# Optimization experiments

Hardware: AMD Instinct MI355X
Metric: run time of the kernel (lower is better)

## Reference

```python
import jax, jax.numpy as jnp
import numpy as np

B, S, P, D, L = 8, 224, 14, 512, 6
NPS = S // P            # 16 patches per side
N = NPS * NPS           # 256 tokens
G = L - 1               # 5 feedforward groups
H = D * 4
TOKEN_ATTEND_SELF_VALUE = -0.0005


def setup_inputs() -> dict:
    key = jax.random.key(0)
    k = jax.random.split(key, 8)
    s = 0.02
    f = jnp.float32
    return {
        "img": jax.random.normal(k[0], (B, 3, S, S), f),
        "W_patch": jax.random.normal(k[1], (P * P * 3, D), f) * s,
        "b_patch": jnp.zeros((D,), f),
        "pos_emb": jax.random.normal(k[2], (N, D), f) * s,
        "init_levels": jax.random.normal(k[3], (L, D), f),
        "bu_W1": jax.random.normal(k[4], (G, D, H), f) * s,
        "bu_b1": jnp.zeros((G, H), f),
        "bu_W2": jax.random.normal(k[5], (G, H, D), f) * s,
        "bu_b2": jnp.zeros((G, D), f),
        "td_W1": jax.random.normal(k[6], (G, D, H), f) * s,
        "td_b1": jnp.zeros((G, H), f),
        "td_W2": jax.random.normal(k[7], (G, H, D), f) * s,
        "td_b2": jnp.zeros((G, D), f),
        "iters": 12,
    }


def _grouped_ff(x, W1, b1, W2, b2):
    # x: [b, n, G, d]; grouped 1x1 conv == independent per-level MLP
    h = jax.nn.gelu(jnp.einsum('bnld,ldh->bnlh', x, W1) + b1, approximate=False)
    return jnp.einsum('bnlh,lhd->bnld', h, W2) + b2


def _consensus(levels):
    # levels: [b, n, L, d]; q = levels, k = l2-normalized levels, v = levels
    d = levels.shape[-1]
    norm = jnp.maximum(jnp.linalg.norm(levels, axis=-1, keepdims=True), 1e-12)
    k = levels / norm
    sim = jnp.einsum('bild,bjld->blij', levels, k) * (d ** -0.5)
    n = levels.shape[1]
    eye = jnp.eye(n, dtype=bool)[None, None]
    sim = jnp.where(eye, TOKEN_ATTEND_SELF_VALUE, sim)  # attend_self=False
    attn = jax.nn.softmax(sim, axis=-1)
    return jnp.einsum('blij,bjld->bild', attn, levels)


def _forward(img, W_patch, b_patch, pos_emb, init_levels,
             bu_W1, bu_b1, bu_W2, bu_b2, td_W1, td_b1, td_W2, td_b2, iters):
    b = img.shape[0]
    # 'b c (h p1) (w p2) -> b (h w) (p1 p2 c)'
    x = img.reshape(b, 3, NPS, P, NPS, P).transpose(0, 2, 4, 3, 5, 1).reshape(b, N, P * P * 3)
    tokens = x @ W_patch + b_patch                  # [b, n, d]
    bottom = tokens[:, :, None, :]                  # [b, n, 1, d]
    levels = jnp.broadcast_to(init_levels, (b, N, L, D)).astype(img.dtype)
    pos = pos_emb[None, :, None, :]
    contrib = jnp.array([4.0] * (L - 1) + [3.0], jnp.float32).reshape(1, 1, L, 1)

    def step(lv, _):
        lw = jnp.concatenate([bottom, lv], axis=-2)                 # [b, n, L+1, d]
        bu = _grouped_ff(lw[..., 1:-1, :], bu_W1, bu_b1, bu_W2, bu_b2)
        td = _grouped_ff(lw[..., 2:, :] + pos, td_W1, td_b1, td_W2, td_b2)
        bu = jnp.concatenate([bottom, bu], axis=-2)                 # [b, n, L, d]
        td = jnp.pad(td, ((0, 0), (0, 0), (0, 1), (0, 0)))          # [b, n, L, d]
        cons = _consensus(lv)
        new = (lv + bu + td + cons) / contrib
        return new, None

    levels, _ = jax.lax.scan(step, levels, None, length=iters)
    return levels


def reference(img, W_patch, b_patch, pos_emb, init_levels,
              bu_W1, bu_b1, bu_W2, bu_b2, td_W1, td_b1, td_W2, td_b2, iters):
    return _forward(img, W_patch, b_patch, pos_emb, init_levels,
                    bu_W1, bu_b1, bu_W2, bu_b2, td_W1, td_b1, td_W2, td_b2, iters)
```

## Files before the change

kernel.cpp:

```cpp
#include <hip/hip_runtime.h>
#include <math.h>

#define L6 6

typedef __attribute__((ext_vector_type(8))) short bf16x8;
typedef __attribute__((ext_vector_type(4))) float f32x4;

#define SH_W_GRP   2097152ull
#define SH_A_TDOFF 10485760ull

__device__ __forceinline__ float gelu_exact(float x) {
  return 0.5f * x * (1.0f + erff(x * 0.70710678118654752f));
}

__device__ __forceinline__ unsigned short bf16_rn(float x) {
  unsigned u = __float_as_uint(x);
  unsigned r = u + 0x7FFFu + ((u >> 16) & 1u);
  return (unsigned short)(r >> 16);
}
__device__ __forceinline__ float bf16_f(unsigned short h) {
  return __uint_as_float(((unsigned)h) << 16);
}
__device__ __forceinline__ void split2(float x, unsigned short* h, unsigned short* l) {
  unsigned short hh = bf16_rn(x);
  *h = hh;
  *l = bf16_rn(x - bf16_f(hh));
}
__device__ __forceinline__ int4 pack8(const unsigned short* v) {
  return make_int4((int)((unsigned)v[0] | ((unsigned)v[1] << 16)),
                   (int)((unsigned)v[2] | ((unsigned)v[3] << 16)),
                   (int)((unsigned)v[4] | ((unsigned)v[5] << 16)),
                   (int)((unsigned)v[6] | ((unsigned)v[7] << 16)));
}

__device__ __forceinline__ void gload16(const void* g, void* l) {
  __builtin_amdgcn_global_load_lds(
      (const __attribute__((address_space(1))) void*)g,
      (__attribute__((address_space(3))) void*)l, 16, 0, 0);
}

__device__ __forceinline__ void patch_embed_body(
    char* smem, const float* __restrict__ img, const float* __restrict__ Wp,
    const float* __restrict__ bp, float* __restrict__ tokens, int bn8)
{
  float (*xs)[588] = (float(*)[588])smem;
  float (*part)[8][4] = (float(*)[8][4])(smem + 18816);
  const int tid = threadIdx.x;
  for (int e = tid; e < 4704; e += 256) {
    int p = e / 588, k = e - p * 588;
    int m = bn8 * 8 + p;
    int b = m >> 8, n = m & 255;
    int i = n >> 4, j = n & 15;
    int c = k % 3;
    int t = k / 3;
    int pc = t % 14;
    int pr = t / 14;
    xs[p][k] = img[(((size_t)(b * 3 + c) * 224) + (i * 14 + pr)) * 224 + (j * 14 + pc)];
  }
  __syncthreads();
  const int kh = tid >> 7, dq = tid & 127, d0 = dq * 4;
  float acc[8][4];
#pragma unroll
  for (int p = 0; p < 8; ++p)
#pragma unroll
    for (int i = 0; i < 4; ++i) acc[p][i] = 0.f;
  const int kbeg = kh * 294;
  for (int k = kbeg; k < kbeg + 294; ++k) {
    float4 wv = *(const float4*)(Wp + (size_t)k * 512 + d0);
#pragma unroll
    for (int p = 0; p < 8; ++p) {
      float x = xs[p][k];
      acc[p][0] = fmaf(x, wv.x, acc[p][0]);
      acc[p][1] = fmaf(x, wv.y, acc[p][1]);
      acc[p][2] = fmaf(x, wv.z, acc[p][2]);
      acc[p][3] = fmaf(x, wv.w, acc[p][3]);
    }
  }
  if (kh == 0) {
#pragma unroll
    for (int p = 0; p < 8; ++p)
      *(float4*)&part[dq][p][0] =
          make_float4(acc[p][0], acc[p][1], acc[p][2], acc[p][3]);
  }
  __syncthreads();
  if (kh == 1) {
    float4 bv = *(const float4*)(bp + d0);
#pragma unroll
    for (int p = 0; p < 8; ++p) {
      int m = bn8 * 8 + p;
      float4 o = make_float4(part[dq][p][0] + acc[p][0] + bv.x,
                             part[dq][p][1] + acc[p][1] + bv.y,
                             part[dq][p][2] + acc[p][2] + bv.z,
                             part[dq][p][3] + acc[p][3] + bv.w);
      *(float4*)(tokens + (size_t)m * 512 + d0) = o;
    }
  }
}

__device__ __forceinline__ void init_lv_body(
    const float* __restrict__ initl, float* __restrict__ lv, int bidx)
{
  int f = bidx * 256 + threadIdx.x;
  int d4 = f & 127;
  int l = (f >> 15) % 6;
  float4 v = *(const float4*)(initl + (size_t)l * 512 + d4 * 4);
  *(float4*)(lv + (size_t)f * 4) = v;
}

__device__ __forceinline__ void pack_w_body(
    const float* __restrict__ src, short* __restrict__ dst, int KT, int NT,
    int inner)
{
  int sidx = inner * 256 + threadIdx.x;
  int slot = sidx & 511;
  int blk = sidx >> 9;
  int kt = blk % KT;
  int rest = blk / KT;
  int nt = rest % NT;
  int g = rest / NT;
  int f = slot >> 6, lane = slot & 63;
  int N = NT * 128, K = KT * 32;
  int n = nt * 128 + f * 16 + (lane & 15);
  int k0 = kt * 32 + (lane >> 4) * 8;
  const float* s = src + ((size_t)g * K + k0) * N + n;
  unsigned short hi[8], lo[8];
#pragma unroll
  for (int j = 0; j < 8; ++j) split2(s[(size_t)j * N], &hi[j], &lo[j]);
  short* d = dst + (size_t)blk * 8192 + slot * 8;
  *(int4*)d = pack8(hi);
  *(int4*)(d + 4096) = pack8(lo);
}

__global__ __launch_bounds__(256) void startup1(
    const float* __restrict__ buW1, const float* __restrict__ tdW1,
    const float* __restrict__ buW2, const float* __restrict__ tdW2,
    short* __restrict__ W1all, short* __restrict__ W2all,
    const float* __restrict__ img, const float* __restrict__ Wp,
    const float* __restrict__ bp, float* __restrict__ tokens,
    const float* __restrict__ initl, float* __restrict__ lv)
{
  __shared__ __align__(16) char smem[35200];
  const int bx = blockIdx.x;
  if (bx < 10240) {
    int q = bx / 2560;
    int inner = bx - q * 2560;
    const float* src = (q == 0) ? buW1 : (q == 1) ? tdW1 : (q == 2) ? buW2 : tdW2;
    short* dst = (q == 0) ? W1all
               : (q == 1) ? W1all + 5 * SH_W_GRP
               : (q == 2) ? W2all
                          : W2all + 5 * SH_W_GRP;
    int KT = (q < 2) ? 16 : 64;
    int NT = (q < 2) ? 16 : 4;
    pack_w_body(src, dst, KT, NT, inner);
  } else if (bx < 10496) {
    patch_embed_body(smem, img, Wp, bp, tokens, bx - 10240);
  } else {
    init_lv_body(initl, lv, bx - 10496);
  }
}

__global__ __launch_bounds__(256) void startup2(
    const float* __restrict__ lv, float* __restrict__ invn,
    const float* __restrict__ pos, short* __restrict__ Abu,
    short* __restrict__ Atd)
{
  if (blockIdx.x < 48) {
    int bl = blockIdx.x;
    int n = threadIdx.x;
    const float* row = lv + ((size_t)bl * 256 + n) * 512;
    float ss = 0.f;
    for (int k = 0; k < 512; k += 4) {
      float4 v = *(const float4*)(row + k);
      ss = fmaf(v.x, v.x, ss);
      ss = fmaf(v.y, v.y, ss);
      ss = fmaf(v.z, v.z, ss);
      ss = fmaf(v.w, v.w, ss);
    }
    invn[(size_t)bl * 256 + n] = 1.0f / fmaxf(sqrtf(ss), 1e-12f);
    return;
  }
  const int bx = blockIdx.x - 48;
  const int lg = bx >> 8, mt = (bx >> 4) & 15, kt = bx & 15;
  const size_t blk = (size_t)bx * 8192;
#pragma unroll
  for (int ss = 0; ss < 2; ++ss) {
    int s = threadIdx.x + ss * 256;
    int f = s >> 6, l = s & 63;
    int m = mt * 128 + (f << 4) + (l & 15);
    int b = m >> 8, n = m & 255;
    int d = kt * 32 + ((l >> 4) << 3);
    const float* pbu = lv + ((size_t)(b * L6 + lg) * 256 + n) * 512 + d;
    const float* ptd = lv + ((size_t)(b * L6 + lg + 1) * 256 + n) * 512 + d;
    const float* pp = pos + (size_t)n * 512 + d;
    float4 u0 = *(const float4*)pbu;
    float4 u1 = *(const float4*)(pbu + 4);
    float xv[8] = {u0.x, u0.y, u0.z, u0.w, u1.x, u1.y, u1.z, u1.w};
    unsigned short hi[8], lo[8];
#pragma unroll
    for (int j = 0; j < 8; ++j) split2(xv[j], &hi[j], &lo[j]);
    *(int4*)(Abu + blk + s * 8) = pack8(hi);
    *(int4*)(Abu + blk + 4096 + s * 8) = pack8(lo);
    float4 v0 = *(const float4*)ptd;
    float4 v1 = *(const float4*)(ptd + 4);
    float4 p0 = *(const float4*)pp;
    float4 p1 = *(const float4*)(pp + 4);
    float yv[8] = {v0.x + p0.x, v0.y + p0.y, v0.z + p0.z, v0.w + p0.w,
                   v1.x + p1.x, v1.y + p1.y, v1.z + p1.z, v1.w + p1.w};
#pragma unroll
    for (int j = 0; j < 8; ++j) split2(yv[j], &hi[j], &lo[j]);
    *(int4*)(Atd + blk + s * 8) = pack8(hi);
    *(int4*)(Atd + blk + 4096 + s * 8) = pack8(lo);
  }
}

__device__ __forceinline__ void ff1_body(
    const short* __restrict__ Wa, const short* __restrict__ Ap,
    const float* __restrict__ b1, short* __restrict__ hpk, int gid)
{
  const int tt = gid & 15;
  const int tile = gid >> 4;
  const int ht = tile & 15;
  const int z = tile >> 4;
  const int tid = threadIdx.x, lane = tid & 63, w = tid >> 6;
  const int wm = (w >> 1) * 64, wn = (w & 1) * 64;
  const short* ga = Wa + (size_t)(z * 16 + ht) * 16 * 8192 + (wm << 5) + lane * 8;
  const short* gb = Ap + (size_t)(z * 16 + tt) * 16 * 8192 + (wn << 5) + lane * 8;

  f32x4 acc[4][4];
#pragma unroll
  for (int i = 0; i < 4; ++i)
#pragma unroll
    for (int j = 0; j < 4; ++j) acc[i][j] = (f32x4)(0.0f);

  for (int kt = 0; kt < 16; ++kt) {
    const short* pa = ga + (size_t)kt * 8192;
    const short* pb = gb + (size_t)kt * 8192;
    bf16x8 ah[4], al[4], bh[4], bl[4];
#pragma unroll
    for (int i = 0; i < 4; ++i) {
      ah[i] = *(const bf16x8*)(pa + i * 512);
      al[i] = *(const bf16x8*)(pa + 4096 + i * 512);
    }
#pragma unroll
    for (int j = 0; j < 4; ++j) {
      bh[j] = *(const bf16x8*)(pb + j * 512);
      bl[j] = *(const bf16x8*)(pb + 4096 + j * 512);
    }
#pragma unroll
    for (int j = 0; j < 4; ++j)
#pragma unroll
      for (int i = 0; i < 4; ++i)
        acc[i][j] = __builtin_amdgcn_mfma_f32_16x16x32_bf16(
            ah[i], bh[j], acc[i][j], 0, 0, 0);
#pragma unroll
    for (int j = 0; j < 4; ++j)
#pragma unroll
      for (int i = 0; i < 4; ++i)
        acc[i][j] = __builtin_amdgcn_mfma_f32_16x16x32_bf16(
            al[i], bh[j], acc[i][j], 0, 0, 0);
#pragma unroll
    for (int j = 0; j < 4; ++j)
#pragma unroll
      for (int i = 0; i < 4; ++i)
        acc[i][j] = __builtin_amdgcn_mfma_f32_16x16x32_bf16(
            ah[i], bl[j], acc[i][j], 0, 0, 0);
  }

  const int q = lane >> 4, t = lane & 15;
  const float* b1g = b1 + (size_t)z * 2048;
#pragma unroll
  for (int i = 0; i < 4; ++i) {
    int Hb = ht * 128 + wm + i * 16 + q * 4;
    float4 bv = *(const float4*)(b1g + Hb);
    float bb[4] = {bv.x, bv.y, bv.z, bv.w};
    int kt2 = Hb >> 5;
    int g2 = (Hb >> 3) & 3;
    int jb = Hb & 7;
    size_t blkbase = ((size_t)(z * 16 + tt) * 64 + kt2) * 4096;
#pragma unroll
    for (int j = 0; j < 4; ++j) {
      int f2 = (wn >> 4) + j;
      size_t off = blkbase + (size_t)(f2 * 64 + g2 * 16 + t) * 8 + jb;
      unsigned short hi[4];
#pragma unroll
      for (int r = 0; r < 4; ++r)
        hi[r] = bf16_rn(gelu_exact(acc[i][j][r] + bb[r]));
      *(uint2*)(hpk + off) =
          make_uint2((unsigned)hi[0] | ((unsigned)hi[1] << 16),
                     (unsigned)hi[2] | ((unsigned)hi[3] << 16));
    }
  }
}

__device__ __forceinline__ void ff2_body(
    char* smem, const short* __restrict__ hpk, const short* __restrict__ Wb,
    const float* __restrict__ b2, const float* __restrict__ lv,
    const float* __restrict__ tokens, float* __restrict__ accum,
    int olvbase, int emode, int gid)
{
  short* SA = (short*)smem;
  short* SB = (short*)(smem + 4096);
  const int nt2 = gid & 3;
  const int tile = gid >> 2;
  const int mt2 = tile & 31;
  const int z = tile >> 5;

  const int tid = threadIdx.x, lane = tid & 63, w = tid >> 6;
  const int wm = (w >> 1) * 32, wn = (w & 1) * 64;
  const short* gaBase = hpk + (size_t)(z * 16 + (mt2 >> 1)) * 64 * 4096
                        + (size_t)(mt2 & 1) * 2048;
  const short* gb = Wb + (size_t)(z * 4 + nt2) * 64 * 8192;

  f32x4 acc[2][4];
#pragma unroll
  for (int i = 0; i < 2; ++i)
#pragma unroll
    for (int j = 0; j < 4; ++j) acc[i][j] = (f32x4)(0.0f);

  for (int kt = 0; kt < 64; ++kt) {
    __syncthreads();
    const char* pa = (const char*)(gaBase + (size_t)kt * 4096);
    const char* pb = (const char*)(gb + (size_t)kt * 8192);
    gload16(pa + w * 1024 + lane * 16, (char*)SA + w * 1024);
#pragma unroll
    for (int c = 0; c < 4; ++c)
      gload16(pb + w * 4096 + c * 1024 + lane * 16,
              (char*)SB + w * 4096 + c * 1024);
    __syncthreads();
    bf16x8 ah[2];
#pragma unroll
    for (int i = 0; i < 2; ++i) {
      int f = (wm >> 4) + i;
      ah[i] = *(const bf16x8*)&SA[f * 512 + lane * 8];
    }
#pragma unroll
    for (int jp = 0; jp < 2; ++jp) {
      bf16x8 bh[2], bl[2];
#pragma unroll
      for (int j2 = 0; j2 < 2; ++j2) {
        int f = (wn >> 4) + jp * 2 + j2;
        bh[j2] = *(const bf16x8*)&SB[f * 512 + lane * 8];
        bl[j2] = *(const bf16x8*)&SB[4096 + f * 512 + lane * 8];
      }
#pragma unroll
      for (int j2 = 0; j2 < 2; ++j2)
#pragma unroll
        for (int i = 0; i < 2; ++i)
          acc[i][jp * 2 + j2] = __builtin_amdgcn_mfma_f32_16x16x32_bf16(
              ah[i], bh[j2], acc[i][jp * 2 + j2], 0, 0, 0);
#pragma unroll
      for (int j2 = 0; j2 < 2; ++j2)
#pragma unroll
        for (int i = 0; i < 2; ++i)
          acc[i][jp * 2 + j2] = __builtin_amdgcn_mfma_f32_16x16x32_bf16(
              ah[i], bl[j2], acc[i][jp * 2 + j2], 0, 0, 0);
    }
  }

  const int q = lane >> 4, t = lane & 15;
  const float* b2g = b2 + (size_t)z * 512;
  const int level = olvbase + z;
#pragma unroll
  for (int i = 0; i < 2; ++i) {
#pragma unroll
    for (int r = 0; r < 4; ++r) {
      int m = mt2 * 64 + wm + i * 16 + q * 4 + r;
      int b = m >> 8, n = m & 255;
      size_t rowoff = ((size_t)(b * L6 + level) * 256 + n) * 512;
      float* arow = accum + rowoff;
      const float* lrow = lv + rowoff;
      const float* trow = tokens + (size_t)m * 512;
#pragma unroll
      for (int j = 0; j < 4; ++j) {
        int col = nt2 * 128 + wn + j * 16 + t;
        float v = acc[i][j][r] + b2g[col];
        if (emode == 0)                       arow[col] = lrow[col] + v;
        else if (level == 0)                  arow[col] = lrow[col] + trow[col] + v;
        else                                  arow[col] += v;
      }
    }
  }
}

__device__ __forceinline__ void attn_body(
    char* smem, const float* __restrict__ lv, const short* __restrict__ Apk,
    const float* __restrict__ invn, float* __restrict__ attnb, int a)
{
  short* Bhi = (short*)smem;
  short* Blo = (short*)(smem + 16384);
  float* scL = (float*)(smem + 32768);
  float (*red)[4] = (float(*)[4])(smem + 33792);
  const int s = a >> 3;
  const int b = a & 7;
  const int l = s >> 3;
  const int bl = b * 6 + l;
  const int i0 = (s & 7) * 32;
  const float* base = lv + (size_t)bl * 131072;
  const int tid = threadIdx.x, lane = tid & 63, w = tid >> 6;
  const int q = lane >> 4, c = lane & 15;

  scL[tid] = invn[(size_t)bl * 256 + tid];

  f32x4 acc[2][4];
#pragma unroll
  for (int i = 0; i < 2; ++i)
#pragma unroll
    for (int j = 0; j < 4; ++j) acc[i][j] = (f32x4)(0.0f);

  const short* src0 = Apk + ((size_t)(l * 16 + 2 * b) * 16) * 8192;
  const short* src1 = Apk + ((size_t)(l * 16 + 2 * b + 1) * 16) * 8192;

  for (int kt = 0; kt < 16; ++kt) {
    __syncthreads();
    if (l < 5) {
      const char* p0 = (const char*)(src0 + (size_t)kt * 8192);
      const char* p1 = (const char*)(src1 + (size_t)kt * 8192);
      gload16(p0 + tid * 16,         (char*)Bhi + tid * 16);
      gload16(p0 + 4096 + tid * 16,  (char*)Bhi + 4096 + tid * 16);
      gload16(p0 + 8192 + tid * 16,  (char*)Blo + tid * 16);
      gload16(p0 + 12288 + tid * 16, (char*)Blo + 4096 + tid * 16);
      gload16(p1 + tid * 16,         (char*)Bhi + 8192 + tid * 16);
      gload16(p1 + 4096 + tid * 16,  (char*)Bhi + 12288 + tid * 16);
      gload16(p1 + 8192 + tid * 16,  (char*)Blo + 8192 + tid * 16);
      gload16(p1 + 12288 + tid * 16, (char*)Blo + 12288 + tid * 16);
    } else {
      const int k0 = kt * 32;
#pragma unroll
      for (int it = 0; it < 8; ++it) {
        int f = it * 256 + tid;
        int j = f >> 3, c4 = f & 7;
        float4 v = *(const float4*)(base + (size_t)j * 512 + k0 + c4 * 4);
        unsigned short hi[4], lo[4];
        split2(v.x, &hi[0], &lo[0]);
        split2(v.y, &hi[1], &lo[1]);
        split2(v.z, &hi[2], &lo[2]);
        split2(v.w, &hi[3], &lo[3]);
        int fg = j >> 4;
        int la = (c4 >> 1) * 16 + (j & 15);
        int half = (c4 & 1) * 4;
        *(uint2*)&Bhi[fg * 512 + la * 8 + half] =
            make_uint2((unsigned)hi[0] | ((unsigned)hi[1] << 16),
                       (unsigned)hi[2] | ((unsigned)hi[3] << 16));
        *(uint2*)&Blo[fg * 512 + la * 8 + half] =
            make_uint2((unsigned)lo[0] | ((unsigned)lo[1] << 16),
                       (unsigned)lo[2] | ((unsigned)lo[3] << 16));
      }
    }
    __syncthreads();
    bf16x8 ah[2], al[2], bh[4], blv[4];
#pragma unroll
    for (int i = 0; i < 2; ++i) {
      int fg = (i0 >> 4) + i;
      ah[i] = *(const bf16x8*)&Bhi[fg * 512 + lane * 8];
      al[i] = *(const bf16x8*)&Blo[fg * 512 + lane * 8];
    }
#pragma unroll
    for (int j = 0; j < 4; ++j) {
      int fg = w * 4 + j;
      bh[j] = *(const bf16x8*)&Bhi[fg * 512 + lane * 8];
      blv[j] = *(const bf16x8*)&Blo[fg * 512 + lane * 8];
    }
#pragma unroll
    for (int j = 0; j < 4; ++j)
#pragma unroll
      for (int i = 0; i < 2; ++i)
        acc[i][j] = __builtin_amdgcn_mfma_f32_16x16x32_bf16(
            ah[i], bh[j], acc[i][j], 0, 0, 0);
#pragma unroll
    for (int j = 0; j < 4; ++j)
#pragma unroll
      for (int i = 0; i < 2; ++i)
        acc[i][j] = __builtin_amdgcn_mfma_f32_16x16x32_bf16(
            al[i], bh[j], acc[i][j], 0, 0, 0);
#pragma unroll
    for (int j = 0; j < 4; ++j)
#pragma unroll
      for (int i = 0; i < 2; ++i)
        acc[i][j] = __builtin_amdgcn_mfma_f32_16x16x32_bf16(
            ah[i], blv[j], acc[i][j], 0, 0, 0);
  }
  __syncthreads();

  const float rs = 0.04419417382415922f;
#pragma unroll
  for (int ai = 0; ai < 2; ++ai)
#pragma unroll
    for (int bj = 0; bj < 4; ++bj)
#pragma unroll
      for (int r = 0; r < 4; ++r) {
        int i = i0 + ai * 16 + q * 4 + r;
        int j = w * 64 + bj * 16 + c;
        float sv = acc[ai][bj][r] * scL[j] * rs;
        if (j == i) sv = -0.0005f;
        acc[ai][bj][r] = sv;
      }
  float mx[2][4];
#pragma unroll
  for (int ai = 0; ai < 2; ++ai)
#pragma unroll
    for (int r = 0; r < 4; ++r) {
      float m = fmaxf(fmaxf(acc[ai][0][r], acc[ai][1][r]),
                      fmaxf(acc[ai][2][r], acc[ai][3][r]));
      m = fmaxf(m, __shfl_xor(m, 1));
      m = fmaxf(m, __shfl_xor(m, 2));
      m = fmaxf(m, __shfl_xor(m, 4));
      m = fmaxf(m, __shfl_xor(m, 8));
      mx[ai][r] = m;
    }
  if (c == 0) {
#pragma unroll
    for (int ai = 0; ai < 2; ++ai)
#pragma unroll
      for (int r = 0; r < 4; ++r) red[ai * 16 + q * 4 + r][w] = mx[ai][r];
  }
  __syncthreads();
#pragma unroll
  for (int ai = 0; ai < 2; ++ai)
#pragma unroll
    for (int r = 0; r < 4; ++r) {
      int row = ai * 16 + q * 4 + r;
      mx[ai][r] = fmaxf(fmaxf(red[row][0], red[row][1]),
                        fmaxf(red[row][2], red[row][3]));
    }
  __syncthreads();
  float sm[2][4];
#pragma unroll
  for (int ai = 0; ai < 2; ++ai)
#pragma unroll
    for (int r = 0; r < 4; ++r) {
      float t = 0.f;
#pragma unroll
      for (int bj = 0; bj < 4; ++bj) {
        float e = expf(acc[ai][bj][r] - mx[ai][r]);
        acc[ai][bj][r] = e;
        t += e;
      }
      t += __shfl_xor(t, 1);
      t += __shfl_xor(t, 2);
      t += __shfl_xor(t, 4);
      t += __shfl_xor(t, 8);
      sm[ai][r] = t;
    }
  if (c == 0) {
#pragma unroll
    for (int ai = 0; ai < 2; ++ai)
#pragma unroll
      for (int r = 0; r < 4; ++r) red[ai * 16 + q * 4 + r][w] = sm[ai][r];
  }
  __syncthreads();
  float* ob = attnb + (size_t)bl * 65536;
#pragma unroll
  for (int ai = 0; ai < 2; ++ai)
#pragma unroll
    for (int r = 0; r < 4; ++r) {
      int row = ai * 16 + q * 4 + r;
      float S = red[row][0] + red[row][1] + red[row][2] + red[row][3];
      float inv = 1.0f / S;
      int i = i0 + row;
#pragma unroll
      for (int bj = 0; bj < 4; ++bj) {
        int j = w * 64 + bj * 16 + c;
        ob[(size_t)i * 256 + j] = acc[ai][bj][r] * inv;
      }
    }
}

__global__ __launch_bounds__(256, 3) void ff1_k(
    const short* __restrict__ Wa, const short* __restrict__ Ap,
    const float* __restrict__ b1, short* __restrict__ hpk)
{
  const int per_x = gridDim.x >> 3;
  const int gid = (blockIdx.x & 7) * per_x + (blockIdx.x >> 3);
  ff1_body(Wa, Ap, b1, hpk, gid);
}

__global__ __launch_bounds__(256, 3) void k_ff2bu_ff1td(
    const short* __restrict__ hallbu, const short* __restrict__ W2,
    const float* __restrict__ bub2, const float* __restrict__ lv,
    const float* __restrict__ tokens, float* __restrict__ accum,
    const short* __restrict__ W1td, const short* __restrict__ Atd,
    const float* __restrict__ tdb1, short* __restrict__ halltd)
{
  __shared__ __align__(16) char smem[20480];
  if (blockIdx.x < 640) {
    int bid = blockIdx.x;
    int gid = (bid & 7) * 80 + (bid >> 3);
    ff2_body(smem, hallbu, W2, bub2, lv, tokens, accum, 1, 0, gid);
  } else {
    int bid = blockIdx.x - 640;
    int gid = (bid & 7) * 160 + (bid >> 3);
    ff1_body(W1td, Atd, tdb1, halltd, gid);
  }
}

__global__ __launch_bounds__(256, 3) void k_ff2td_attn(
    const short* __restrict__ halltd, const short* __restrict__ W2td,
    const float* __restrict__ tdb2, const float* __restrict__ lv,
    const float* __restrict__ tokens, float* __restrict__ accum,
    const short* __restrict__ Apk, const float* __restrict__ invn,
    float* __restrict__ attnb)
{
  __shared__ __align__(16) char smem[34304];
  if (blockIdx.x < 640) {
    int bid = blockIdx.x;
    int gid = (bid & 7) * 80 + (bid >> 3);
    ff2_body(smem, halltd, W2td, tdb2, lv, tokens, accum, 0, 1, gid);
  } else {
    attn_body(smem, lv, Apk, invn, attnb, blockIdx.x - 640);
  }
}

__global__ __launch_bounds__(256) void cons_k(
    const float* __restrict__ attnb, const float* __restrict__ lv,
    float* __restrict__ accum)
{
  __shared__ __align__(16) char smemraw[25088];
  const int a = blockIdx.x;
  const int s = a >> 3;
  const int bl = (a & 7) * 6 + (s >> 4);
  const int tile = s & 15;
  int it0 = (tile >> 2) * 64;
  int dt0 = (tile & 3) * 128;
  const float* A = attnb + (size_t)bl * 65536;
  const float* Bm = lv + (size_t)bl * 131072;
  float (*Ast)[68] = (float(*)[68])smemraw;
  float (*Bs)[128] = (float(*)[128])(smemraw + 8704);
  const int tid = threadIdx.x;
  const int ty = tid >> 4, tx = tid & 15;
  float acc[4][8];
#pragma unroll
  for (int i = 0; i < 4; ++i)
#pragma unroll
    for (int j = 0; j < 8; ++j) acc[i][j] = 0.f;

  for (int k0 = 0; k0 < 256; k0 += 32) {
#pragma unroll
    for (int it = 0; it < 2; ++it) {
      int f = it * 256 + tid;
      int r = f >> 3, c4 = f & 7;
      float4 v = *(const float4*)(A + (size_t)(it0 + r) * 256 + k0 + c4 * 4);
      Ast[c4 * 4 + 0][r] = v.x;
      Ast[c4 * 4 + 1][r] = v.y;
      Ast[c4 * 4 + 2][r] = v.z;
      Ast[c4 * 4 + 3][r] = v.w;
    }
#pragma unroll
    for (int it = 0; it < 4; ++it) {
      int kr = (tid >> 5) + it * 8;
      int c4 = tid & 31;
      *(float4*)&Bs[kr][c4 * 4] =
          *(const float4*)(Bm + (size_t)(k0 + kr) * 512 + dt0 + c4 * 4);
    }
    __syncthreads();
#pragma unroll 8
    for (int k = 0; k < 32; ++k) {
      float4 av = *(const float4*)&Ast[k][ty * 4];
      float4 b0 = *(const float4*)&Bs[k][tx * 4];
      float4 b1 = *(const float4*)&Bs[k][64 + tx * 4];
      float avv[4] = {av.x, av.y, av.z, av.w};
      float bv[8] = {b0.x, b0.y, b0.z, b0.w, b1.x, b1.y, b1.z, b1.w};
#pragma unroll
      for (int i = 0; i < 4; ++i)
#pragma unroll
        for (int j = 0; j < 8; ++j)
          acc[i][j] = fmaf(avv[i], bv[j], acc[i][j]);
    }
    __syncthreads();
  }
#pragma unroll
  for (int ii = 0; ii < 4; ++ii) {
    int i = it0 + ty * 4 + ii;
    float* arow = accum + (size_t)bl * 131072 + (size_t)i * 512 + dt0;
#pragma unroll
    for (int j = 0; j < 4; ++j) arow[tx * 4 + j] += acc[ii][j];
#pragma unroll
    for (int j = 0; j < 4; ++j) arow[64 + tx * 4 + j] += acc[ii][4 + j];
  }
}

__global__ __launch_bounds__(256) void combine3(
    const float* __restrict__ accum, const float* __restrict__ pos,
    float* __restrict__ lv_out, short* __restrict__ Abu,
    short* __restrict__ Atd, float* __restrict__ invn,
    float* __restrict__ dout, int last)
{
  int t = blockIdx.x * 256 + threadIdx.x;
  int d8 = t & 63;
  int n = (t >> 6) & 255;
  int v = t >> 14;
  int l = v % 6, b = v / 6;
  int bn = (b << 8) | n;
  size_t idx = ((size_t)v * 256 + n) * 512 + d8 * 8;
  float4 a0 = *(const float4*)(accum + idx);
  float4 a1 = *(const float4*)(accum + idx + 4);
  float sc = (l == 5) ? (1.0f / 3.0f) : 0.25f;
  float r[8];
  r[0] = a0.x * sc; r[1] = a0.y * sc; r[2] = a0.z * sc; r[3] = a0.w * sc;
  r[4] = a1.x * sc; r[5] = a1.y * sc; r[6] = a1.z * sc; r[7] = a1.w * sc;
  *(float4*)(lv_out + idx) = make_float4(r[0], r[1], r[2], r[3]);
  *(float4*)(lv_out + idx + 4) = make_float4(r[4], r[5], r[6], r[7]);
  if (last) {
    float* dp = dout + ((size_t)bn * 6 + l) * 512 + d8 * 8;
    *(float4*)dp = make_float4(r[0], r[1], r[2], r[3]);
    *(float4*)(dp + 4) = make_float4(r[4], r[5], r[6], r[7]);
  }
  {
    float s8 = 0.f;
#pragma unroll
    for (int j = 0; j < 8; ++j) s8 = fmaf(r[j], r[j], s8);
#pragma unroll
    for (int o = 1; o < 64; o <<= 1) s8 += __shfl_xor(s8, o);
    if (d8 == 0) invn[(size_t)v * 256 + n] = 1.0f / fmaxf(sqrtf(s8), 1e-12f);
  }
  int m = bn;
  int mt = m >> 7;
  int kt = d8 >> 2;
  int s = (((m & 127) >> 4) << 6) | (((d8 & 3) << 4) | (m & 15));
  unsigned short hi[8], lo[8];
  if (l < 5) {
    size_t blk = ((size_t)(l * 16 + mt) * 16 + kt) * 8192;
#pragma unroll
    for (int j = 0; j < 8; ++j) split2(r[j], &hi[j], &lo[j]);
    *(int4*)(Abu + blk + s * 8) = pack8(hi);
    *(int4*)(Abu + blk + 4096 + s * 8) = pack8(lo);
  }
  if (l >= 1) {
    const float* pp = pos + (size_t)n * 512 + d8 * 8;
    float4 p0 = *(const float4*)pp;
    float4 p1 = *(const float4*)(pp + 4);
    float y[8] = {r[0] + p0.x, r[1] + p0.y, r[2] + p0.z, r[3] + p0.w,
                  r[4] + p1.x, r[5] + p1.y, r[6] + p1.z, r[7] + p1.w};
    size_t blk = ((size_t)((l - 1) * 16 + mt) * 16 + kt) * 8192;
#pragma unroll
    for (int j = 0; j < 8; ++j) split2(y[j], &hi[j], &lo[j]);
    *(int4*)(Atd + blk + s * 8) = pack8(hi);
    *(int4*)(Atd + blk + 4096 + s * 8) = pack8(lo);
  }
}

extern "C" void kernel_launch(void* const* d_in, const int* in_sizes, int n_in,
                              void* d_out, int out_size, void* d_ws, size_t ws_size,
                              hipStream_t stream)
{
  const float* img   = (const float*)d_in[0];
  const float* Wp    = (const float*)d_in[1];
  const float* bp    = (const float*)d_in[2];
  const float* pos   = (const float*)d_in[3];
  const float* initl = (const float*)d_in[4];
  const float* buW1  = (const float*)d_in[5];
  const float* bub1  = (const float*)d_in[6];
  const float* buW2  = (const float*)d_in[7];
  const float* bub2  = (const float*)d_in[8];
  const float* tdW1  = (const float*)d_in[9];
  const float* tdb1  = (const float*)d_in[10];
  const float* tdW2  = (const float*)d_in[11];
  const float* tdb2  = (const float*)d_in[12];

  float* ws = (float*)d_ws;
  const size_t LV = (size_t)8 * 6 * 256 * 512;
  float* lv     = ws;
  float* tokens = lv + LV;
  float* accum  = tokens + 1048576ull;
  short* W1all  = (short*)(accum + LV);
  short* W2all  = W1all + 20971520ull;
  short* Apk    = W2all + 20971520ull;
  short* hallbu = Apk + 20971520ull;
  short* halltd = hallbu + 20971520ull;
  float* invn   = (float*)(halltd + 20971520ull);

  float* attnb = (float*)hallbu;
  float* dout  = (float*)d_out;

  startup1<<<16640, 256, 0, stream>>>(buW1, tdW1, buW2, tdW2, W1all, W2all,
                                      img, Wp, bp, tokens, initl, lv);
  startup2<<<1328, 256, 0, stream>>>(lv, invn, pos, Apk, Apk + SH_A_TDOFF);

  for (int it = 0; it < 12; ++it) {
    ff1_k<<<1280, 256, 0, stream>>>(W1all, Apk, bub1, hallbu);
    k_ff2bu_ff1td<<<1920, 256, 0, stream>>>(
        hallbu, W2all, bub2, lv, tokens, accum,
        W1all + 5 * SH_W_GRP, Apk + SH_A_TDOFF, tdb1, halltd);
    k_ff2td_attn<<<1024, 256, 0, stream>>>(
        halltd, W2all + 5 * SH_W_GRP, tdb2, lv, tokens, accum,
        Apk, invn, attnb);
    cons_k<<<768, 256, 0, stream>>>(attnb, lv, accum);
    combine3<<<3072, 256, 0, stream>>>(accum, pos, lv, Apk, Apk + SH_A_TDOFF,
                                       invn, dout, it == 11 ? 1 : 0);
  }
}
```

Baseline: 3.915 ms.

## Re-slice per-iteration kernels into six diagonal stages mixing levels across phases

Splits each iteration's work into six launches where different level groups run at different phases: bu FF1 for levels 0-2, then FF1 for levels 3-4 together with FF2 for levels 0-1 and td FF1, and so on through consensus and combine. The goal is to balance block counts per launch and overlap compute-heavy GEMMs with memory-bound consensus and combine work, shrinking idle tails. The cost is one more launch per iteration, plus correctness that depends on a subtle cross-level dependency ordering. For example, combine for some levels runs while consensus for others is still pending, and it overwrites lv and Abu/Atd that later stages read.

```diff
diff --git a/kernel.cpp b/kernel.cpp
--- a/kernel.cpp
+++ b/kernel.cpp
@@ -215,12 +215,12 @@
 
 __device__ __forceinline__ void ff1_body(
     const short* __restrict__ Wa, const short* __restrict__ Ap,
-    const float* __restrict__ b1, short* __restrict__ hpk, int gid)
+    const float* __restrict__ b1, short* __restrict__ hpk, int gid, int zoff)
 {
   const int tt = gid & 15;
   const int tile = gid >> 4;
   const int ht = tile & 15;
-  const int z = tile >> 4;
+  const int z = zoff + (tile >> 4);
   const int tid = threadIdx.x, lane = tid & 63, w = tid >> 6;
   const int wm = (w >> 1) * 64, wn = (w & 1) * 64;
   const short* ga = Wa + (size_t)(z * 16 + ht) * 16 * 8192 + (wm << 5) + lane * 8;
@@ -296,14 +296,14 @@
     char* smem, const short* __restrict__ hpk, const short* __restrict__ Wb,
     const float* __restrict__ b2, const float* __restrict__ lv,
     const float* __restrict__ tokens, float* __restrict__ accum,
-    int olvbase, int emode, int gid)
+    int olvbase, int emode, int gid, int zoff)
 {
   short* SA = (short*)smem;
   short* SB = (short*)(smem + 4096);
   const int nt2 = gid & 3;
   const int tile = gid >> 2;
   const int mt2 = tile & 31;
-  const int z = tile >> 5;
+  const int z = zoff + (tile >> 5);
 
   const int tid = threadIdx.x, lane = tid & 63, w = tid >> 6;
   const int wm = (w >> 1) * 32, wn = (w & 1) * 64;
@@ -565,66 +565,16 @@
     }
 }
 
-__global__ __launch_bounds__(256, 3) void ff1_k(
-    const short* __restrict__ Wa, const short* __restrict__ Ap,
-    const float* __restrict__ b1, short* __restrict__ hpk)
-{
-  const int per_x = gridDim.x >> 3;
-  const int gid = (blockIdx.x & 7) * per_x + (blockIdx.x >> 3);
-  ff1_body(Wa, Ap, b1, hpk, gid);
-}
-
-__global__ __launch_bounds__(256, 3) void k_ff2bu_ff1td(
-    const short* __restrict__ hallbu, const short* __restrict__ W2,
-    const float* __restrict__ bub2, const float* __restrict__ lv,
-    const float* __restrict__ tokens, float* __restrict__ accum,
-    const short* __restrict__ W1td, const short* __restrict__ Atd,
-    const float* __restrict__ tdb1, short* __restrict__ halltd)
-{
-  __shared__ __align__(16) char smem[20480];
-  if (blockIdx.x < 640) {
-    int bid = blockIdx.x;
-    int gid = (bid & 7) * 80 + (bid >> 3);
-    ff2_body(smem, hallbu, W2, bub2, lv, tokens, accum, 1, 0, gid);
-  } else {
-    int bid = blockIdx.x - 640;
-    int gid = (bid & 7) * 160 + (bid >> 3);
-    ff1_body(W1td, Atd, tdb1, halltd, gid);
-  }
-}
-
-__global__ __launch_bounds__(256, 3) void k_ff2td_attn(
-    const short* __restrict__ halltd, const short* __restrict__ W2td,
-    const float* __restrict__ tdb2, const float* __restrict__ lv,
-    const float* __restrict__ tokens, float* __restrict__ accum,
-    const short* __restrict__ Apk, const float* __restrict__ invn,
-    float* __restrict__ attnb)
-{
-  __shared__ __align__(16) char smem[34304];
-  if (blockIdx.x < 640) {
-    int bid = blockIdx.x;
-    int gid = (bid & 7) * 80 + (bid >> 3);
-    ff2_body(smem, halltd, W2td, tdb2, lv, tokens, accum, 0, 1, gid);
-  } else {
-    attn_body(smem, lv, Apk, invn, attnb, blockIdx.x - 640);
-  }
-}
-
-__global__ __launch_bounds__(256) void cons_k(
-    const float* __restrict__ attnb, const float* __restrict__ lv,
-    float* __restrict__ accum)
-{
-  __shared__ __align__(16) char smemraw[25088];
-  const int a = blockIdx.x;
-  const int s = a >> 3;
-  const int bl = (a & 7) * 6 + (s >> 4);
-  const int tile = s & 15;
+__device__ __forceinline__ void cons_body(
+    char* smem, const float* __restrict__ attnb, const float* __restrict__ lv,
+    float* __restrict__ accum, int bl, int tile)
+{
   int it0 = (tile >> 2) * 64;
   int dt0 = (tile & 3) * 128;
   const float* A = attnb + (size_t)bl * 65536;
   const float* Bm = lv + (size_t)bl * 131072;
-  float (*Ast)[68] = (float(*)[68])smemraw;
-  float (*Bs)[128] = (float(*)[128])(smemraw + 8704);
+  float (*Ast)[68] = (float(*)[68])smem;
+  float (*Bs)[128] = (float(*)[128])(smem + 8704);
   const int tid = threadIdx.x;
   const int ty = tid >> 4, tx = tid & 15;
   float acc[4][8];
@@ -678,17 +628,16 @@
   }
 }
 
-__global__ __launch_bounds__(256) void combine3(
+__device__ __forceinline__ void combine_body(
     const float* __restrict__ accum, const float* __restrict__ pos,
     float* __restrict__ lv_out, short* __restrict__ Abu,
     short* __restrict__ Atd, float* __restrict__ invn,
-    float* __restrict__ dout, int last)
-{
-  int t = blockIdx.x * 256 + threadIdx.x;
-  int d8 = t & 63;
-  int n = (t >> 6) & 255;
-  int v = t >> 14;
-  int l = v % 6, b = v / 6;
+    float* __restrict__ dout, int last, int b, int l, int inner)
+{
+  int f = inner * 256 + threadIdx.x;
+  int d8 = f & 63;
+  int n = f >> 6;
+  int v = b * 6 + l;
   int bn = (b << 8) | n;
   size_t idx = ((size_t)v * 256 + n) * 512 + d8 * 8;
   float4 a0 = *(const float4*)(accum + idx);
@@ -738,6 +687,124 @@
   }
 }
 
+__global__ __launch_bounds__(256, 3) void k_d1(
+    const short* __restrict__ W1bu, const short* __restrict__ Abu,
+    const float* __restrict__ bub1, short* __restrict__ hallbu)
+{
+  const int gid = (blockIdx.x & 7) * 96 + (blockIdx.x >> 3);
+  ff1_body(W1bu, Abu, bub1, hallbu, gid, 0);
+}
+
+__global__ __launch_bounds__(256, 3) void k_d2(
+    const short* __restrict__ W1bu, const short* __restrict__ Abu,
+    const float* __restrict__ bub1, short* __restrict__ hallbu,
+    const short* __restrict__ W2bu, const float* __restrict__ bub2,
+    const float* __restrict__ lv, const float* __restrict__ tokens,
+    float* __restrict__ accum,
+    const short* __restrict__ W1td, const short* __restrict__ Atd,
+    const float* __restrict__ tdb1, short* __restrict__ halltd)
+{
+  __shared__ __align__(16) char smem[20480];
+  const int bx = blockIdx.x;
+  if (bx < 512) {
+    int gid = (bx & 7) * 64 + (bx >> 3);
+    ff1_body(W1bu, Abu, bub1, hallbu, gid, 3);
+  } else if (bx < 768) {
+    int a = bx - 512;
+    int gid = (a & 7) * 32 + (a >> 3);
+    ff2_body(smem, hallbu, W2bu, bub2, lv, tokens, accum, 1, 0, gid, 0);
+  } else {
+    int a = bx - 768;
+    int gid = (a & 7) * 160 + (a >> 3);
+    ff1_body(W1td, Atd, tdb1, halltd, gid, 0);
+  }
+}
+
+__global__ __launch_bounds__(256, 3) void k_d3(
+    const short* __restrict__ hallbu, const short* __restrict__ W2bu,
+    const float* __restrict__ bub2,
+    const short* __restrict__ halltd, const short* __restrict__ W2td,
+    const float* __restrict__ tdb2,
+    const float* __restrict__ lv, const float* __restrict__ tokens,
+    float* __restrict__ accum,
+    const short* __restrict__ Apk, const float* __restrict__ invn,
+    float* __restrict__ attnb)
+{
+  __shared__ __align__(16) char smem[34304];
+  const int bx = blockIdx.x;
+  if (bx < 384) {
+    int gid = (bx & 7) * 48 + (bx >> 3);
+    ff2_body(smem, hallbu, W2bu, bub2, lv, tokens, accum, 1, 0, gid, 2);
+  } else if (bx < 768) {
+    int a = bx - 384;
+    int gid = (a & 7) * 48 + (a >> 3);
+    ff2_body(smem, halltd, W2td, tdb2, lv, tokens, accum, 0, 1, gid, 0);
+  } else {
+    attn_body(smem, lv, Apk, invn, attnb, bx - 768);
+  }
+}
+
+__global__ __launch_bounds__(256, 3) void k_d4(
+    const short* __restrict__ halltd, const short* __restrict__ W2td,
+    const float* __restrict__ tdb2, const float* __restrict__ lv,
+    const float* __restrict__ tokens, float* __restrict__ accum,
+    const float* __restrict__ attnb)
+{
+  __shared__ __align__(16) char smem[25088];
+  const int bx = blockIdx.x;
+  if (bx < 256) {
+    int gid = (bx & 7) * 32 + (bx >> 3);
+    ff2_body(smem, halltd, W2td, tdb2, lv, tokens, accum, 0, 1, gid, 3);
+  } else {
+    int a = bx - 256;
+    int s = a >> 3;
+    int li = s >> 4;
+    int l = (li == 3) ? 5 : li;
+    int bl = (a & 7) * 6 + l;
+    cons_body(smem, attnb, lv, accum, bl, s & 15);
+  }
+}
+
+__global__ __launch_bounds__(256, 3) void k_d5(
+    const float* __restrict__ attnb, const float* __restrict__ lv,
+    float* __restrict__ accum,
+    const float* __restrict__ pos, float* __restrict__ lv_out,
+    short* __restrict__ Abu, short* __restrict__ Atd,
+    float* __restrict__ invn, float* __restrict__ dout, int last)
+{
+  __shared__ __align__(16) char smem[25088];
+  const int bx = blockIdx.x;
+  if (bx < 256) {
+    int a = bx;
+    int s = a >> 3;
+    int l = 3 + (s >> 4);
+    int bl = (a & 7) * 6 + l;
+    cons_body(smem, attnb, lv, accum, bl, s & 15);
+  } else {
+    int u = bx - 256;
+    int vb = u >> 6;
+    int inner = u & 63;
+    int b = vb >> 2;
+    int li = vb & 3;
+    int l = (li == 3) ? 5 : li;
+    combine_body(accum, pos, lv_out, Abu, Atd, invn, dout, last, b, l, inner);
+  }
+}
+
+__global__ __launch_bounds__(256) void k_d6(
+    const float* __restrict__ accum, const float* __restrict__ pos,
+    float* __restrict__ lv_out, short* __restrict__ Abu,
+    short* __restrict__ Atd, float* __restrict__ invn,
+    float* __restrict__ dout, int last)
+{
+  int u = blockIdx.x;
+  int vb = u >> 6;
+  int inner = u & 63;
+  int b = vb >> 1;
+  int l = 3 + (vb & 1);
+  combine_body(accum, pos, lv_out, Abu, Atd, invn, dout, last, b, l, inner);
+}
+
 extern "C" void kernel_launch(void* const* d_in, const int* in_sizes, int n_in,
                               void* d_out, int out_size, void* d_ws, size_t ws_size,
                               hipStream_t stream)
@@ -775,16 +842,27 @@
                                       img, Wp, bp, tokens, initl, lv);
   startup2<<<1328, 256, 0, stream>>>(lv, invn, pos, Apk, Apk + SH_A_TDOFF);
 
+  const short* W1bu = W1all;
+  const short* W1td = W1all + 5 * SH_W_GRP;
+  const short* W2bu = W2all;
+  const short* W2td = W2all + 5 * SH_W_GRP;
+  const short* Abu = Apk;
+  const short* Atd = Apk + SH_A_TDOFF;
+
   for (int it = 0; it < 12; ++it) {
-    ff1_k<<<1280, 256, 0, stream>>>(W1all, Apk, bub1, hallbu);
-    k_ff2bu_ff1td<<<1920, 256, 0, stream>>>(
-        hallbu, W2all, bub2, lv, tokens, accum,
-        W1all + 5 * SH_W_GRP, Apk + SH_A_TDOFF, tdb1, halltd);
-    k_ff2td_attn<<<1024, 256, 0, stream>>>(
-        halltd, W2all + 5 * SH_W_GRP, tdb2, lv, tokens, accum,
-        Apk, invn, attnb);
-    cons_k<<<768, 256, 0, stream>>>(attnb, lv, accum);
-    combine3<<<3072, 256, 0, stream>>>(accum, pos, lv, Apk, Apk + SH_A_TDOFF,
-                                       invn, dout, it == 11 ? 1 : 0);
-  }
-}
+    int last = (it == 11) ? 1 : 0;
+    k_d1<<<768, 256, 0, stream>>>(W1bu, Abu, bub1, hallbu);
+    k_d2<<<2048, 256, 0, stream>>>(W1bu, Abu, bub1, hallbu,
+                                   W2bu, bub2, lv, tokens, accum,
+                                   W1td, Atd, tdb1, halltd);
+    k_d3<<<1152, 256, 0, stream>>>(hallbu, W2bu, bub2,
+                                   halltd, W2td, tdb2,
+                                   lv, tokens, accum, Apk, invn, attnb);
+    k_d4<<<768, 256, 0, stream>>>(halltd, W2td, tdb2, lv, tokens, accum,
+                                  attnb);
+    k_d5<<<2304, 256, 0, stream>>>(attnb, lv, accum, pos, lv,
+                                   (short*)Abu, (short*)Atd, invn, dout, last);
+    k_d6<<<1024, 256, 0, stream>>>(accum, pos, lv, (short*)Abu, (short*)Atd,
+                                   invn, dout, last);
+  }
+}
```

New measurement: 4.328 ms. 10.5% more time.
